# Performance work log

Hardware: AMD Instinct MI355X
Metric: run time of the kernel (lower is better)

The kernel has to match this reference:

```python
import jax, jax.numpy as jnp
import numpy as np

N = 100000
E = 1600000
F_NODE = 6
F_EDGE = 2
H = 64


def _glorot(key, shape):
    lim = float(np.sqrt(6.0 / (shape[0] + shape[1])))
    return jax.random.uniform(key, shape, jnp.float32, -lim, lim)


def setup_inputs() -> dict:
    key = jax.random.key(0)
    ks = jax.random.split(key, 16)
    inp = {
        "x": jax.random.normal(ks[0], (N, F_NODE), jnp.float32),
        "edge_index": jax.random.randint(ks[1], (2, E), 0, N, jnp.int64),
        "edge_attr": jax.random.normal(ks[2], (E, F_EDGE), jnp.float32),
        # GCN layers (PyG GCNConv: linear no-bias, then aggregate, then +bias)
        "W1": _glorot(ks[3], (F_NODE, H)), "b1": jnp.zeros((H,), jnp.float32),
        "W2": _glorot(ks[4], (H, H)), "b2": jnp.zeros((H,), jnp.float32),
        "W3": _glorot(ks[5], (H, H)), "b3": jnp.zeros((H,), jnp.float32),
        # edge_mlp
        "We1": _glorot(ks[6], (F_EDGE, H)), "be1": jnp.zeros((H,), jnp.float32),
        "We2": _glorot(ks[7], (H, H)), "be2": jnp.zeros((H,), jnp.float32),
        # predictor
        "Wp1": _glorot(ks[8], (3 * H, H)), "bp1": jnp.zeros((H,), jnp.float32),
        "Wp2": _glorot(ks[9], (H, H // 2)), "bp2": jnp.zeros((H // 2,), jnp.float32),
        "Wp3": _glorot(ks[10], (H // 2, 1)), "bp3": jnp.zeros((1,), jnp.float32),
    }
    return inp


def _gcn_conv(h, W, b, src_sl, dst_sl, norm, n):
    # PyG GCNConv with self-loops and symmetric normalization
    h = h @ W                                   # [N, H_out]
    msg = h[src_sl] * norm[:, None]             # gather + scale per edge(+loop)
    out = jax.ops.segment_sum(msg, dst_sl, num_segments=n)
    return out + b


def _forward(x, edge_attr, W1, b1, W2, b2, W3, b3, We1, be1, We2, be2,
             Wp1, bp1, Wp2, bp2, Wp3, bp3, edge_index):
    n = x.shape[0]
    src, dst = edge_index[0], edge_index[1]

    # --- edge feature injection (vectorized version of per-edge loop) ---
    ef = jax.nn.relu(edge_attr @ We1 + be1) @ We2 + be2      # [E, H]
    nef = (jax.ops.segment_sum(ef, src, num_segments=n)
           + jax.ops.segment_sum(ef, dst, num_segments=n))   # [N, H]
    ones_e = jnp.ones((ef.shape[0],), x.dtype)
    deg = (jax.ops.segment_sum(ones_e, src, num_segments=n)
           + jax.ops.segment_sum(ones_e, dst, num_segments=n))
    deg = jnp.maximum(deg, 1.0)
    nef = nef / deg[:, None]
    # hidden_dim (64) >= node feature dim (6) -> truncate
    x = x + nef[:, : x.shape[1]] * 0.5

    # --- GCN normalization with self-loops (shared across layers) ---
    loop = jnp.arange(n, dtype=src.dtype)
    src_sl = jnp.concatenate([src, loop])
    dst_sl = jnp.concatenate([dst, loop])
    deg_sl = jax.ops.segment_sum(jnp.ones_like(dst_sl, dtype=x.dtype), dst_sl,
                                 num_segments=n)
    dinv = jnp.where(deg_sl > 0, deg_sl ** -0.5, 0.0)
    norm = dinv[src_sl] * dinv[dst_sl]

    h = jax.nn.relu(_gcn_conv(x, W1, b1, src_sl, dst_sl, norm, n))
    h = jax.nn.relu(_gcn_conv(h, W2, b2, src_sl, dst_sl, norm, n))
    h = _gcn_conv(h, W3, b3, src_sl, dst_sl, norm, n)

    graph_emb = h.mean(axis=0)                 # global_mean_pool, batch=None
    node_mean = h.mean(axis=0)
    node_std = jnp.std(h, axis=0, ddof=1)      # torch.std is unbiased
    combined = jnp.concatenate([graph_emb, node_mean, node_std])  # [3H]

    p = jax.nn.relu(combined @ Wp1 + bp1)      # dropout inactive in eval
    p = jax.nn.relu(p @ Wp2 + bp2)
    out = jax.nn.sigmoid(p @ Wp3 + bp3)        # (1,)
    return out


def reference(x, edge_index, edge_attr, W1, b1, W2, b2, W3, b3,
              We1, be1, We2, be2, Wp1, bp1, Wp2, bp2, Wp3, bp3):
    return _forward(x, edge_attr, W1, b1, W2, b2, W3, b3, We1, be1, We2, be2,
                    Wp1, bp1, Wp2, bp2, Wp3, bp3, edge_index)
```

## Files before the change

kernel.cpp:

```cpp
#include <hip/hip_runtime.h>
#include <hip/hip_bf16.h>
#include <stdint.h>

__device__ __forceinline__ float rdlane(float v, int l) {
    return __uint_as_float(__builtin_amdgcn_readlane(__float_as_uint(v), l));
}
__device__ __forceinline__ float bf2f(unsigned short u) {
    return __uint_as_float(((unsigned)u) << 16);
}
__device__ __forceinline__ unsigned short f2bf(float f) {
    unsigned u = __float_as_uint(f);
    u += 0x7fffu + ((u >> 16) & 1u);
    return (unsigned short)(u >> 16);
}
__device__ __forceinline__ unsigned packbf(float a, float b) {
    return (unsigned)f2bf(a) | ((unsigned)f2bf(b) << 16);
}

__global__ void k_zero(int* __restrict__ cntO, int* __restrict__ cntI,
                       double* __restrict__ sums, int n) {
    int i = blockIdx.x * blockDim.x + threadIdx.x;
    if (i < 128) sums[i] = 0.0;
    if (i < n) { cntO[i] = 0; cntI[i] = 0; }
}

__global__ __launch_bounds__(256) void k_front(
    const int* __restrict__ ei, const float* __restrict__ ea,
    const float* __restrict__ We1, const float* __restrict__ be1,
    const float* __restrict__ We2, const float* __restrict__ be2,
    unsigned* __restrict__ efp, int* __restrict__ cntO, int* __restrict__ cntI,
    int* __restrict__ rankS, int* __restrict__ rankD, int E) {
    __shared__ float sWe1[128], sbe1[64], sWe2[64 * 6], sbe2[6];
    int t = threadIdx.x;
    if (t < 128) sWe1[t] = We1[t];
    if (t < 64) {
        sbe1[t] = be1[t];
#pragma unroll
        for (int c = 0; c < 6; ++c) sWe2[t * 6 + c] = We2[t * 64 + c];
    }
    if (t < 6) sbe2[t] = be2[t];
    __syncthreads();

    int e = blockIdx.x * blockDim.x + t;
    if (e >= E) return;

    int s = ei[e], d = ei[E + e];
    int rs = atomicAdd(&cntO[s], 1);
    int rd = atomicAdd(&cntI[d], 1);

    float a0 = ea[2 * e], a1 = ea[2 * e + 1];
    float acc[6];
#pragma unroll
    for (int c = 0; c < 6; ++c) acc[c] = sbe2[c];
#pragma unroll
    for (int j = 0; j < 64; ++j) {
        float h = fmaf(a0, sWe1[j], fmaf(a1, sWe1[64 + j], sbe1[j]));
        h = fmaxf(h, 0.f);
#pragma unroll
        for (int c = 0; c < 6; ++c) acc[c] = fmaf(h, sWe2[j * 6 + c], acc[c]);
    }
    unsigned* q = efp + (size_t)e * 3;
    q[0] = packbf(acc[0], acc[1]);
    q[1] = packbf(acc[2], acc[3]);
    q[2] = packbf(acc[4], acc[5]);
    rankS[e] = rs;
    rankD[e] = rd;
}

__global__ __launch_bounds__(256) void k_scan1(const int* __restrict__ cnt,
                                               int* __restrict__ bsum, int n) {
    __shared__ int l[256];
    int i = blockIdx.x * 256 + threadIdx.x;
    l[threadIdx.x] = (i < n) ? cnt[i] : 0;
    __syncthreads();
    for (int s = 128; s > 0; s >>= 1) {
        if (threadIdx.x < s) l[threadIdx.x] += l[threadIdx.x + s];
        __syncthreads();
    }
    if (threadIdx.x == 0) bsum[blockIdx.x] = l[0];
}

__global__ __launch_bounds__(512) void k_scan2(int* __restrict__ bsum, int nb,
                                               int* __restrict__ offN) {
    __shared__ int l[512];
    int t = threadIdx.x;
    int v = (t < nb) ? bsum[t] : 0;
    l[t] = v;
    __syncthreads();
    for (int s = 1; s < 512; s <<= 1) {
        int tmp = (t >= s) ? l[t - s] : 0;
        __syncthreads();
        l[t] += tmp;
        __syncthreads();
    }
    if (t < nb) bsum[t] = l[t] - v;
    if (t == 511) *offN = l[511];
}

__global__ __launch_bounds__(256) void k_scan3off(const int* __restrict__ cnt,
                                                  const int* __restrict__ bsum,
                                                  int* __restrict__ off, int n) {
    __shared__ int l[256];
    int i = blockIdx.x * 256 + threadIdx.x;
    int v = (i < n) ? cnt[i] : 0;
    l[threadIdx.x] = v;
    __syncthreads();
    for (int s = 1; s < 256; s <<= 1) {
        int tmp = (threadIdx.x >= (unsigned)s) ? l[threadIdx.x - s] : 0;
        __syncthreads();
        l[threadIdx.x] += tmp;
        __syncthreads();
    }
    if (i < n) off[i] = l[threadIdx.x] - v + bsum[blockIdx.x];
}

__global__ __launch_bounds__(256) void k_place(const int* __restrict__ ei,
                                               const int* __restrict__ rankS,
                                               const int* __restrict__ rankD,
                                               const int* __restrict__ offO,
                                               const int* __restrict__ offI,
                                               unsigned* __restrict__ out_eid,
                                               uint2* __restrict__ in_pk, int E) {
    int e = blockIdx.x * blockDim.x + threadIdx.x;
    if (e >= E) return;
    int s = ei[e], d = ei[E + e];
    out_eid[offO[s] + rankS[e]] = (unsigned)e;
    in_pk[offI[d] + rankD[e]] = make_uint2((unsigned)s, (unsigned)e);
}

__global__ __launch_bounds__(256) void k_nef_x(
    const int* __restrict__ offO, const unsigned* __restrict__ out_eid,
    const int* __restrict__ offI, const uint2* __restrict__ in_pk,
    const unsigned* __restrict__ efp, const float* __restrict__ x,
    float* __restrict__ xp, float* __restrict__ dinv, int n) {
    int i = blockIdx.x * blockDim.x + threadIdx.x;
    if (i >= n) return;
    int bo = offO[i], eo = offO[i + 1];
    int bi = offI[i], eiN = offI[i + 1];
    float a0 = 0.f, a1 = 0.f, a2 = 0.f, a3 = 0.f, a4 = 0.f, a5 = 0.f;
    for (int j = bo; j < eo; ++j) {
        const unsigned* q = efp + (size_t)out_eid[j] * 3;
        unsigned u0 = q[0], u1 = q[1], u2 = q[2];
        a0 += bf2f((unsigned short)u0); a1 += bf2f((unsigned short)(u0 >> 16));
        a2 += bf2f((unsigned short)u1); a3 += bf2f((unsigned short)(u1 >> 16));
        a4 += bf2f((unsigned short)u2); a5 += bf2f((unsigned short)(u2 >> 16));
    }
    for (int j = bi; j < eiN; ++j) {
        const unsigned* q = efp + (size_t)in_pk[j].y * 3;
        unsigned u0 = q[0], u1 = q[1], u2 = q[2];
        a0 += bf2f((unsigned short)u0); a1 += bf2f((unsigned short)(u0 >> 16));
        a2 += bf2f((unsigned short)u1); a3 += bf2f((unsigned short)(u1 >> 16));
        a4 += bf2f((unsigned short)u2); a5 += bf2f((unsigned short)(u2 >> 16));
    }
    int indeg = eiN - bi;
    float degf = (float)((eo - bo) + indeg);
    float inv = 0.5f / fmaxf(degf, 1.f);
    xp[(size_t)i * 6 + 0] = x[(size_t)i * 6 + 0] + a0 * inv;
    xp[(size_t)i * 6 + 1] = x[(size_t)i * 6 + 1] + a1 * inv;
    xp[(size_t)i * 6 + 2] = x[(size_t)i * 6 + 2] + a2 * inv;
    xp[(size_t)i * 6 + 3] = x[(size_t)i * 6 + 3] + a3 * inv;
    xp[(size_t)i * 6 + 4] = x[(size_t)i * 6 + 4] + a4 * inv;
    xp[(size_t)i * 6 + 5] = x[(size_t)i * 6 + 5] + a5 * inv;
    dinv[i] = 1.f / sqrtf(1.f + (float)indeg);
}

__global__ __launch_bounds__(256) void k_mm1(const float* __restrict__ xp,
                                             const float* __restrict__ W1,
                                             const float* __restrict__ dinv,
                                             unsigned short* __restrict__ sOut, int n) {
    int lane = threadIdx.x & 63;
    int wid = (blockIdx.x * blockDim.x + threadIdx.x) >> 6;
    int nw = (gridDim.x * blockDim.x) >> 6;
    float w[6];
#pragma unroll
    for (int c = 0; c < 6; ++c) w[c] = W1[c * 64 + lane];
    for (int i = wid; i < n; i += nw) {
        float xv = (lane < 6) ? xp[(size_t)i * 6 + lane] : 0.f;
        float acc = 0.f;
#pragma unroll
        for (int c = 0; c < 6; ++c) acc = fmaf(rdlane(xv, c), w[c], acc);
        sOut[(size_t)i * 64 + lane] = f2bf(acc * dinv[i]);
    }
}

__global__ __launch_bounds__(256) void k_gathermm(
    const int* __restrict__ offI, const uint2* __restrict__ in_pk,
    const float* __restrict__ dinv, const unsigned short* __restrict__ sIn,
    const float* __restrict__ bias, const float* __restrict__ W,
    unsigned short* __restrict__ sOut, int n) {
    int lane = threadIdx.x & 63;
    int sub = lane & 15, grp = lane >> 4;
    int wid = (blockIdx.x * blockDim.x + threadIdx.x) >> 6;
    int nw = (gridDim.x * blockDim.x) >> 6;
    float w[64];
#pragma unroll
    for (int c = 0; c < 64; ++c) w[c] = W[c * 64 + lane];
    float4 bb = ((const float4*)bias)[sub];

    for (int i = wid; i < n; i += nw) {
        ushort4 sv = *(const ushort4*)(sIn + (size_t)i * 64 + sub * 4);
        float a0, a1, a2, a3;
        if (grp == 0) { a0 = bf2f(sv.x); a1 = bf2f(sv.y); a2 = bf2f(sv.z); a3 = bf2f(sv.w); }
        else { a0 = a1 = a2 = a3 = 0.f; }
        int b0 = offI[i], e0 = offI[i + 1];
#pragma unroll 2
        for (int j = b0 + grp; j < e0; j += 4) {
            unsigned src = in_pk[j].x;
            ushort4 v = *(const ushort4*)(sIn + (size_t)src * 64 + sub * 4);
            a0 += bf2f(v.x); a1 += bf2f(v.y); a2 += bf2f(v.z); a3 += bf2f(v.w);
        }
        a0 += __shfl_xor(a0, 16); a1 += __shfl_xor(a1, 16);
        a2 += __shfl_xor(a2, 16); a3 += __shfl_xor(a3, 16);
        a0 += __shfl_xor(a0, 32); a1 += __shfl_xor(a1, 32);
        a2 += __shfl_xor(a2, 32); a3 += __shfl_xor(a3, 32);

        float dv = dinv[i];
        float h0 = fmaxf(fmaf(a0, dv, bb.x), 0.f);
        float h1 = fmaxf(fmaf(a1, dv, bb.y), 0.f);
        float h2 = fmaxf(fmaf(a2, dv, bb.z), 0.f);
        float h3 = fmaxf(fmaf(a3, dv, bb.w), 0.f);
        float o = 0.f;
#pragma unroll
        for (int g = 0; g < 16; ++g) {
            o = fmaf(rdlane(h0, g), w[g * 4 + 0], o);
            o = fmaf(rdlane(h1, g), w[g * 4 + 1], o);
            o = fmaf(rdlane(h2, g), w[g * 4 + 2], o);
            o = fmaf(rdlane(h3, g), w[g * 4 + 3], o);
        }
        sOut[(size_t)i * 64 + lane] = f2bf(o * dv);
    }
}

__global__ __launch_bounds__(256) void k_gatherreduce(
    const int* __restrict__ offI, const uint2* __restrict__ in_pk,
    const float* __restrict__ dinv, const unsigned short* __restrict__ sIn,
    const float* __restrict__ b3, double* __restrict__ sums, int n) {
    int lane = threadIdx.x & 63;
    int sub = lane & 15, grp = lane >> 4;
    int wv = threadIdx.x >> 6;
    int wid = (blockIdx.x * blockDim.x + threadIdx.x) >> 6;
    int nw = (gridDim.x * blockDim.x) >> 6;
    float4 bb = ((const float4*)b3)[sub];
    double s0 = 0.0, s1 = 0.0, s2_ = 0.0, s3 = 0.0;
    double q0 = 0.0, q1 = 0.0, q2 = 0.0, q3 = 0.0;

    for (int i = wid; i < n; i += nw) {
        ushort4 sv = *(const ushort4*)(sIn + (size_t)i * 64 + sub * 4);
        float a0, a1, a2, a3;
        if (grp == 0) { a0 = bf2f(sv.x); a1 = bf2f(sv.y); a2 = bf2f(sv.z); a3 = bf2f(sv.w); }
        else { a0 = a1 = a2 = a3 = 0.f; }
        int b0 = offI[i], e0 = offI[i + 1];
#pragma unroll 2
        for (int j = b0 + grp; j < e0; j += 4) {
            unsigned src = in_pk[j].x;
            ushort4 v = *(const ushort4*)(sIn + (size_t)src * 64 + sub * 4);
            a0 += bf2f(v.x); a1 += bf2f(v.y); a2 += bf2f(v.z); a3 += bf2f(v.w);
        }
        a0 += __shfl_xor(a0, 16); a1 += __shfl_xor(a1, 16);
        a2 += __shfl_xor(a2, 16); a3 += __shfl_xor(a3, 16);
        a0 += __shfl_xor(a0, 32); a1 += __shfl_xor(a1, 32);
        a2 += __shfl_xor(a2, 32); a3 += __shfl_xor(a3, 32);

        float dv = dinv[i];
        float v0 = fmaf(a0, dv, bb.x);
        float v1 = fmaf(a1, dv, bb.y);
        float v2 = fmaf(a2, dv, bb.z);
        float v3 = fmaf(a3, dv, bb.w);
        s0 += v0; s1 += v1; s2_ += v2; s3 += v3;
        q0 += (double)v0 * v0; q1 += (double)v1 * v1;
        q2 += (double)v2 * v2; q3 += (double)v3 * v3;
    }
    __shared__ double shS[4 * 64], shQ[4 * 64];
    if (grp == 0) {
#pragma unroll
        for (int k = 0; k < 4; ++k) {
            double sk = (k == 0) ? s0 : (k == 1) ? s1 : (k == 2) ? s2_ : s3;
            double qk = (k == 0) ? q0 : (k == 1) ? q1 : (k == 2) ? q2 : q3;
            shS[wv * 64 + sub * 4 + k] = sk;
            shQ[wv * 64 + sub * 4 + k] = qk;
        }
    }
    __syncthreads();
    if (wv == 0) {
        double a = shS[lane] + shS[64 + lane] + shS[128 + lane] + shS[192 + lane];
        double c = shQ[lane] + shQ[64 + lane] + shQ[128 + lane] + shQ[192 + lane];
        unsafeAtomicAdd(&sums[lane], a);
        unsafeAtomicAdd(&sums[64 + lane], c);
    }
}

__global__ void k_head(const double* __restrict__ sums,
                       const float* __restrict__ Wp1, const float* __restrict__ bp1,
                       const float* __restrict__ Wp2, const float* __restrict__ bp2,
                       const float* __restrict__ Wp3, const float* __restrict__ bp3,
                       float* __restrict__ out, int n) {
    __shared__ float comb[192], p1[64], p2[32];
    int t = threadIdx.x;
    if (t < 64) {
        double s = sums[t], s2 = sums[64 + t];
        double m = s / n;
        double var = (s2 - s * s / n) / (double)(n - 1);
        float mf = (float)m;
        float sd = (float)sqrt(var > 0.0 ? var : 0.0);
        comb[t] = mf;
        comb[64 + t] = mf;
        comb[128 + t] = sd;
    }
    __syncthreads();
    if (t < 64) {
        float acc = bp1[t];
        for (int k = 0; k < 192; ++k) acc = fmaf(comb[k], Wp1[k * 64 + t], acc);
        p1[t] = fmaxf(acc, 0.f);
    }
    __syncthreads();
    if (t < 32) {
        float acc = bp2[t];
        for (int k = 0; k < 64; ++k) acc = fmaf(p1[k], Wp2[k * 32 + t], acc);
        p2[t] = fmaxf(acc, 0.f);
    }
    __syncthreads();
    if (t == 0) {
        float acc = bp3[0];
        for (int k = 0; k < 32; ++k) acc = fmaf(p2[k], Wp3[k], acc);
        out[0] = 1.f / (1.f + expf(-acc));
    }
}

static inline char* align16(char* p) {
    return (char*)(((uintptr_t)p + 15) & ~(uintptr_t)15);
}

extern "C" void kernel_launch(void* const* d_in, const int* in_sizes, int n_in,
                              void* d_out, int out_size, void* d_ws, size_t ws_size,
                              hipStream_t stream) {
    const float* x   = (const float*)d_in[0];
    const int*   ei  = (const int*)d_in[1];
    const float* ea  = (const float*)d_in[2];
    const float* W1  = (const float*)d_in[3];
    const float* b1  = (const float*)d_in[4];
    const float* W2  = (const float*)d_in[5];
    const float* b2  = (const float*)d_in[6];
    const float* W3  = (const float*)d_in[7];
    const float* b3  = (const float*)d_in[8];
    const float* We1 = (const float*)d_in[9];
    const float* be1 = (const float*)d_in[10];
    const float* We2 = (const float*)d_in[11];
    const float* be2 = (const float*)d_in[12];
    const float* Wp1 = (const float*)d_in[13];
    const float* bp1 = (const float*)d_in[14];
    const float* Wp2 = (const float*)d_in[15];
    const float* bp2 = (const float*)d_in[16];
    const float* Wp3 = (const float*)d_in[17];
    const float* bp3 = (const float*)d_in[18];

    const int N = in_sizes[0] / 6;
    const int E = in_sizes[1] / 2;
    const int nbN = (N + 255) / 256;
    const int nbE = (E + 255) / 256;
    const size_t SB = (size_t)N * 64 * 2;

    char* p = (char*)d_ws;
    double* sums = (double*)p;          p = align16(p + 128 * sizeof(double));
    int* cntO = (int*)p;                p = align16(p + (size_t)N * 4);
    int* cntI = (int*)p;                p = align16(p + (size_t)N * 4);
    int* offO = (int*)p;                p = align16(p + ((size_t)N + 1) * 4);
    int* offI = (int*)p;                p = align16(p + ((size_t)N + 1) * 4);
    int* bsumA = (int*)p;               p = align16(p + 512 * 4);
    int* bsumB = (int*)p;               p = align16(p + 512 * 4);
    float* xp = (float*)p;              p = align16(p + (size_t)N * 6 * 4);
    float* dinv = (float*)p;            p = align16(p + (size_t)N * 4);
    uint2* in_pk = (uint2*)p;           p = align16(p + (size_t)E * 8);
    char* u1 = p;                       p = align16(p + 2 * SB);
    int* rankS = (int*)u1;
    int* rankD = (int*)(u1 + SB);
    unsigned short* sbufA = (unsigned short*)u1;
    unsigned short* sbufB = (unsigned short*)(u1 + SB);
    char* u2 = p;
    unsigned* efp = (unsigned*)u2;
    unsigned* out_eid = (unsigned*)(u2 + (size_t)E * 12);

    const int TB = 256;
    dim3 blk(TB);

    k_zero<<<dim3(nbN), blk, 0, stream>>>(cntO, cntI, sums, N);
    k_front<<<dim3(nbE), blk, 0, stream>>>(ei, ea, We1, be1, We2, be2,
                                           efp, cntO, cntI, rankS, rankD, E);
    k_scan1<<<dim3(nbN), blk, 0, stream>>>(cntO, bsumA, N);
    k_scan1<<<dim3(nbN), blk, 0, stream>>>(cntI, bsumB, N);
    k_scan2<<<dim3(1), dim3(512), 0, stream>>>(bsumA, nbN, offO + N);
    k_scan2<<<dim3(1), dim3(512), 0, stream>>>(bsumB, nbN, offI + N);
    k_scan3off<<<dim3(nbN), blk, 0, stream>>>(cntO, bsumA, offO, N);
    k_scan3off<<<dim3(nbN), blk, 0, stream>>>(cntI, bsumB, offI, N);
    k_place<<<dim3(nbE), blk, 0, stream>>>(ei, rankS, rankD, offO, offI, out_eid, in_pk, E);
    k_nef_x<<<dim3(nbN), blk, 0, stream>>>(offO, out_eid, offI, in_pk, efp, x, xp, dinv, N);

    k_mm1<<<dim3(1024), blk, 0, stream>>>(xp, W1, dinv, sbufA, N);
    k_gathermm<<<dim3(2048), blk, 0, stream>>>(offI, in_pk, dinv, sbufA, b1, W2, sbufB, N);
    k_gathermm<<<dim3(2048), blk, 0, stream>>>(offI, in_pk, dinv, sbufB, b2, W3, sbufA, N);
    k_gatherreduce<<<dim3(2048), blk, 0, stream>>>(offI, in_pk, dinv, sbufA, b3, sums, N);
    k_head<<<dim3(1), dim3(64), 0, stream>>>(sums, Wp1, bp1, Wp2, bp2, Wp3, bp3,
                                             (float*)d_out, N);
}
```

Before: 585.9 us.

## Pad degree counters, fuse dual scans, vectorize edge-attr load, unroll gathers more

Degree counters are spread out to one per 32 bytes so that atomics on neighbouring nodes no longer contend on the same cache line. The separate out-degree and in-degree scan kernels are merged into int2 versions, cutting three launches. The edge-attribute read becomes a single float2 load, and the gather loops in the GCN kernels are unrolled 4 instead of 2 to keep more loads in flight. The trade-off is that the strided counters use eight times the workspace and give uncoalesced reads in the scan kernels.

```diff
diff --git a/kernel.cpp b/kernel.cpp
--- a/kernel.cpp
+++ b/kernel.cpp
@@ -1,6 +1,8 @@
 #include <hip/hip_runtime.h>
 #include <hip/hip_bf16.h>
 #include <stdint.h>
+
+#define CSTRIDE 8
 
 __device__ __forceinline__ float rdlane(float v, int l) {
     return __uint_as_float(__builtin_amdgcn_readlane(__float_as_uint(v), l));
@@ -21,7 +23,7 @@
                        double* __restrict__ sums, int n) {
     int i = blockIdx.x * blockDim.x + threadIdx.x;
     if (i < 128) sums[i] = 0.0;
-    if (i < n) { cntO[i] = 0; cntI[i] = 0; }
+    if (i < n) { cntO[(size_t)i * CSTRIDE] = 0; cntI[(size_t)i * CSTRIDE] = 0; }
 }
 
 __global__ __launch_bounds__(256) void k_front(
@@ -45,10 +47,11 @@
     if (e >= E) return;
 
     int s = ei[e], d = ei[E + e];
-    int rs = atomicAdd(&cntO[s], 1);
-    int rd = atomicAdd(&cntI[d], 1);
-
-    float a0 = ea[2 * e], a1 = ea[2 * e + 1];
+    int rs = atomicAdd(&cntO[(size_t)s * CSTRIDE], 1);
+    int rd = atomicAdd(&cntI[(size_t)d * CSTRIDE], 1);
+
+    float2 aa = ((const float2*)ea)[e];
+    float a0 = aa.x, a1 = aa.y;
     float acc[6];
 #pragma unroll
     for (int c = 0; c < 6; ++c) acc[c] = sbe2[c];
@@ -67,51 +70,66 @@
     rankD[e] = rd;
 }
 
-__global__ __launch_bounds__(256) void k_scan1(const int* __restrict__ cnt,
-                                               int* __restrict__ bsum, int n) {
-    __shared__ int l[256];
+__global__ __launch_bounds__(256) void k_scan1(const int* __restrict__ cntO,
+                                               const int* __restrict__ cntI,
+                                               int2* __restrict__ bsum, int n) {
+    __shared__ int2 l[256];
     int i = blockIdx.x * 256 + threadIdx.x;
-    l[threadIdx.x] = (i < n) ? cnt[i] : 0;
+    l[threadIdx.x] = (i < n) ? make_int2(cntO[(size_t)i * CSTRIDE],
+                                         cntI[(size_t)i * CSTRIDE])
+                             : make_int2(0, 0);
     __syncthreads();
     for (int s = 128; s > 0; s >>= 1) {
-        if (threadIdx.x < s) l[threadIdx.x] += l[threadIdx.x + s];
+        if (threadIdx.x < s) {
+            l[threadIdx.x].x += l[threadIdx.x + s].x;
+            l[threadIdx.x].y += l[threadIdx.x + s].y;
+        }
         __syncthreads();
     }
     if (threadIdx.x == 0) bsum[blockIdx.x] = l[0];
 }
 
-__global__ __launch_bounds__(512) void k_scan2(int* __restrict__ bsum, int nb,
-                                               int* __restrict__ offN) {
-    __shared__ int l[512];
+__global__ __launch_bounds__(512) void k_scan2(int2* __restrict__ bsum, int nb,
+                                               int* __restrict__ offON,
+                                               int* __restrict__ offIN) {
+    __shared__ int2 l[512];
     int t = threadIdx.x;
-    int v = (t < nb) ? bsum[t] : 0;
+    int2 v = (t < nb) ? bsum[t] : make_int2(0, 0);
     l[t] = v;
     __syncthreads();
     for (int s = 1; s < 512; s <<= 1) {
-        int tmp = (t >= s) ? l[t - s] : 0;
+        int2 tmp = (t >= s) ? l[t - s] : make_int2(0, 0);
         __syncthreads();
-        l[t] += tmp;
+        l[t].x += tmp.x; l[t].y += tmp.y;
         __syncthreads();
     }
-    if (t < nb) bsum[t] = l[t] - v;
-    if (t == 511) *offN = l[511];
-}
-
-__global__ __launch_bounds__(256) void k_scan3off(const int* __restrict__ cnt,
-                                                  const int* __restrict__ bsum,
-                                                  int* __restrict__ off, int n) {
-    __shared__ int l[256];
+    if (t < nb) bsum[t] = make_int2(l[t].x - v.x, l[t].y - v.y);
+    if (t == 511) { *offON = l[511].x; *offIN = l[511].y; }
+}
+
+__global__ __launch_bounds__(256) void k_scan3off(const int* __restrict__ cntO,
+                                                  const int* __restrict__ cntI,
+                                                  const int2* __restrict__ bsum,
+                                                  int* __restrict__ offO,
+                                                  int* __restrict__ offI, int n) {
+    __shared__ int2 l[256];
     int i = blockIdx.x * 256 + threadIdx.x;
-    int v = (i < n) ? cnt[i] : 0;
+    int2 v = (i < n) ? make_int2(cntO[(size_t)i * CSTRIDE],
+                                 cntI[(size_t)i * CSTRIDE])
+                     : make_int2(0, 0);
     l[threadIdx.x] = v;
     __syncthreads();
     for (int s = 1; s < 256; s <<= 1) {
-        int tmp = (threadIdx.x >= (unsigned)s) ? l[threadIdx.x - s] : 0;
+        int2 tmp = (threadIdx.x >= (unsigned)s) ? l[threadIdx.x - s] : make_int2(0, 0);
         __syncthreads();
-        l[threadIdx.x] += tmp;
+        l[threadIdx.x].x += tmp.x; l[threadIdx.x].y += tmp.y;
         __syncthreads();
     }
-    if (i < n) off[i] = l[threadIdx.x] - v + bsum[blockIdx.x];
+    if (i < n) {
+        int2 bs = bsum[blockIdx.x];
+        offO[i] = l[threadIdx.x].x - v.x + bs.x;
+        offI[i] = l[threadIdx.x].y - v.y + bs.y;
+    }
 }
 
 __global__ __launch_bounds__(256) void k_place(const int* __restrict__ ei,
@@ -203,7 +221,7 @@
         if (grp == 0) { a0 = bf2f(sv.x); a1 = bf2f(sv.y); a2 = bf2f(sv.z); a3 = bf2f(sv.w); }
         else { a0 = a1 = a2 = a3 = 0.f; }
         int b0 = offI[i], e0 = offI[i + 1];
-#pragma unroll 2
+#pragma unroll 4
         for (int j = b0 + grp; j < e0; j += 4) {
             unsigned src = in_pk[j].x;
             ushort4 v = *(const ushort4*)(sIn + (size_t)src * 64 + sub * 4);
@@ -250,7 +268,7 @@
         if (grp == 0) { a0 = bf2f(sv.x); a1 = bf2f(sv.y); a2 = bf2f(sv.z); a3 = bf2f(sv.w); }
         else { a0 = a1 = a2 = a3 = 0.f; }
         int b0 = offI[i], e0 = offI[i + 1];
-#pragma unroll 2
+#pragma unroll 4
         for (int j = b0 + grp; j < e0; j += 4) {
             unsigned src = in_pk[j].x;
             ushort4 v = *(const ushort4*)(sIn + (size_t)src * 64 + sub * 4);
@@ -361,12 +379,11 @@
 
     char* p = (char*)d_ws;
     double* sums = (double*)p;          p = align16(p + 128 * sizeof(double));
-    int* cntO = (int*)p;                p = align16(p + (size_t)N * 4);
-    int* cntI = (int*)p;                p = align16(p + (size_t)N * 4);
+    int* cntO = (int*)p;                p = align16(p + (size_t)N * CSTRIDE * 4);
+    int* cntI = (int*)p;                p = align16(p + (size_t)N * CSTRIDE * 4);
     int* offO = (int*)p;                p = align16(p + ((size_t)N + 1) * 4);
     int* offI = (int*)p;                p = align16(p + ((size_t)N + 1) * 4);
-    int* bsumA = (int*)p;               p = align16(p + 512 * 4);
-    int* bsumB = (int*)p;               p = align16(p + 512 * 4);
+    int2* bsum = (int2*)p;              p = align16(p + 512 * 8);
     float* xp = (float*)p;              p = align16(p + (size_t)N * 6 * 4);
     float* dinv = (float*)p;            p = align16(p + (size_t)N * 4);
     uint2* in_pk = (uint2*)p;           p = align16(p + (size_t)E * 8);
@@ -385,12 +402,9 @@
     k_zero<<<dim3(nbN), blk, 0, stream>>>(cntO, cntI, sums, N);
     k_front<<<dim3(nbE), blk, 0, stream>>>(ei, ea, We1, be1, We2, be2,
                                            efp, cntO, cntI, rankS, rankD, E);
-    k_scan1<<<dim3(nbN), blk, 0, stream>>>(cntO, bsumA, N);
-    k_scan1<<<dim3(nbN), blk, 0, stream>>>(cntI, bsumB, N);
-    k_scan2<<<dim3(1), dim3(512), 0, stream>>>(bsumA, nbN, offO + N);
-    k_scan2<<<dim3(1), dim3(512), 0, stream>>>(bsumB, nbN, offI + N);
-    k_scan3off<<<dim3(nbN), blk, 0, stream>>>(cntO, bsumA, offO, N);
-    k_scan3off<<<dim3(nbN), blk, 0, stream>>>(cntI, bsumB, offI, N);
+    k_scan1<<<dim3(nbN), blk, 0, stream>>>(cntO, cntI, bsum, N);
+    k_scan2<<<dim3(1), dim3(512), 0, stream>>>(bsum, nbN, offO + N, offI + N);
+    k_scan3off<<<dim3(nbN), blk, 0, stream>>>(cntO, cntI, bsum, offO, offI, N);
     k_place<<<dim3(nbE), blk, 0, stream>>>(ei, rankS, rankD, offO, offI, out_eid, in_pk, E);
     k_nef_x<<<dim3(nbN), blk, 0, stream>>>(offO, out_eid, offI, in_pk, efp, x, xp, dinv, N);
 
```

After: 593.9 us. No clear change (+1.4%).
